# Kernel optimization log

Hardware: AMD Instinct MI355X
Metric: run time of the kernel (lower is better)

Reference implementation:

```python
import jax, jax.numpy as jnp
import numpy as np

# --- fixed physical constants (module params are requires_grad=False) ---
G = 9.81
M = 0.1667
CAF = 5.0 * 0.25 * M * G          # tanh(0) -> ratio = 1.0 exactly
CAR = CAF
LF = 0.09 - 0.036
LR = 0.036
IZ = 0.000267                      # tanh(0) -> pow_ratio = 0 -> Iz_base
THROTTLE_OFFSET = 0.24
THROTTLE_RATIO = 6.98
DT = 0.01
RES_BOUNDS = jnp.array([0.05 * G, 0.05 * G, 0.05 * G * 0.2], dtype=jnp.float32)

B, H, T = 131072, 4, 32


def setup_inputs() -> dict:
    key = jax.random.key(0)
    ks = jax.random.split(key, 8)
    # realistic car states: [x, vx_w, y, vy_w, psi, yaw_rate]
    pos = jax.random.normal(ks[0], (B, H, 2)) * 1.0
    vx = 2.0 + 0.2 * jax.random.normal(ks[1], (B, H, 1))
    vy = 0.1 * jax.random.normal(ks[2], (B, H, 1))
    psi = 0.2 * jax.random.normal(ks[3], (B, H, 1))
    r = 0.1 * jax.random.normal(ks[4], (B, H, 1))
    thr = 0.30 + 0.05 * jax.random.normal(ks[5], (B, H, 1))
    steer = 0.05 * jax.random.normal(ks[6], (B, H, 1))
    full_states = jnp.concatenate(
        [pos[..., :1], vx, pos[..., 1:], vy, psi, r, thr, steer], axis=-1
    ).astype(jnp.float32)
    ka = jax.random.split(ks[7], 6)
    actions = jnp.concatenate(
        [0.30 + 0.05 * jax.random.normal(ka[0], (B, T, 1)),
         0.05 * jax.random.normal(ka[1], (B, T, 1))], axis=-1).astype(jnp.float32)
    in_dim = H * 8
    fc1_w = (jax.random.normal(ka[2], (16, in_dim)) / np.sqrt(in_dim)).astype(jnp.float32)
    fc1_b = (0.01 * jax.random.normal(ka[3], (16,))).astype(jnp.float32)
    fc2_w = (jax.random.normal(ka[4], (3, 16)) / np.sqrt(16)).astype(jnp.float32)
    fc2_b = (0.01 * jax.random.normal(ka[5], (3,))).astype(jnp.float32)
    return {"full_states": full_states, "actions": actions,
            "fc1_w": fc1_w, "fc1_b": fc1_b, "fc2_w": fc2_w, "fc2_b": fc2_b,
            "enable_rnn": 1}


def _rollout(full_states, actions, fc1_w, fc1_b, fc2_w, fc2_b, enable_rnn):
    bsz = full_states.shape[0]
    a33 = lambda Vx: -(2 * CAF + 2 * CAR) / (M * Vx)
    a35 = lambda Vx: -Vx - (2 * CAF * LF - 2 * CAR * LR) / (M * Vx)
    a53 = lambda Vx: -(2 * LF * CAF - 2 * LR * CAR) / (IZ * Vx)
    a55 = lambda Vx: -(2 * LF ** 2 * CAF + 2 * LR ** 2 * CAR) / (IZ * Vx)

    def step(window, act):  # window [B,H,8], act [B,2]
        s = window[:, -1, :6]
        thr, steer = window[:, -1, 6], window[:, -1, 7]
        psi = s[:, 4]
        c, sn = jnp.cos(psi), jnp.sin(psi)
        Vx = s[:, 1] * c + s[:, 3] * sn
        # v = R(-psi) @ s  (body frame)
        v1 = c * s[:, 1] + sn * s[:, 3]
        v3 = -sn * s[:, 1] + c * s[:, 3]
        v5 = s[:, 5]
        long_acc = (thr - THROTTLE_OFFSET) * THROTTLE_RATIO
        # d = A @ v + B @ u
        d0 = v1
        d1 = long_acc
        d2 = v3
        d3 = a33(Vx) * v3 + a35(Vx) * v5 + (2 * CAF / M) * steer
        d4 = v5
        d5 = a53(Vx) * v3 + a55(Vx) * v5 + (2 * LF * CAF / IZ) * steer
        if enable_rnn:
            flat = window.reshape(bsz, -1)
            y1 = jnp.tanh(flat @ fc1_w.T + fc1_b)
            y2 = jnp.tanh(y1 @ fc2_w.T + fc2_b) * RES_BOUNDS[None, :]
            d1 = d1 + y2[:, 0] / M
            d3 = d3 + y2[:, 1] / M
            d5 = d5 + y2[:, 2] / IZ
        # s_new = s + R(psi) @ d * dt
        ns0 = s[:, 0] + (c * d0 - sn * d2) * DT
        ns1 = s[:, 1] + (c * d1 - sn * d3) * DT
        ns2 = s[:, 2] + (sn * d0 + c * d2) * DT
        ns3 = s[:, 3] + (sn * d1 + c * d3) * DT
        ns4 = jnp.mod(s[:, 4] + d4 * DT + jnp.pi, 2 * jnp.pi) - jnp.pi
        ns5 = s[:, 5] + d5 * DT
        new_full = jnp.stack([ns0, ns1, ns2, ns3, ns4, ns5, act[:, 0], act[:, 1]], axis=1)
        new_window = jnp.concatenate([window[:, 1:], new_full[:, None, :]], axis=1)
        return new_window, new_full

    acts_t = jnp.swapaxes(actions, 0, 1)  # [T,B,2]
    _, outs = jax.lax.scan(step, full_states, acts_t)
    return jnp.swapaxes(outs, 0, 1)  # [B,T,8]


def reference(full_states, actions, fc1_w, fc1_b, fc2_w, fc2_b, enable_rnn):
    return _rollout(full_states, actions, fc1_w, fc1_b, fc2_w, fc2_b, bool(enable_rnn))
```

## Files before the change

### kernel.cpp

```cpp
#include <hip/hip_runtime.h>
#include <math.h>

namespace {

typedef short  bf16x8 __attribute__((ext_vector_type(8)));
typedef float  f32x4  __attribute__((ext_vector_type(4)));

constexpr int B_TOTAL = 131072;
constexpr int T_STEPS = 32;

constexpr double dG   = 9.81;
constexpr double dM   = 0.1667;
constexpr double dCAF = 5.0 * 0.25 * dM * dG;
constexpr double dCAR = dCAF;
constexpr double dLF  = 0.09 - 0.036;
constexpr double dLR  = 0.036;
constexpr double dIZ  = 0.000267;

constexpr float A33N = (float)(-(2.0 * dCAF + 2.0 * dCAR));
constexpr float A35N = (float)(-(2.0 * dCAF * dLF - 2.0 * dCAR * dLR));
constexpr float A53N = (float)(-(2.0 * dLF * dCAF - 2.0 * dLR * dCAR));
constexpr float A55N = (float)(-(2.0 * dLF * dLF * dCAF + 2.0 * dLR * dLR * dCAR));
constexpr float ST1  = (float)(2.0 * dCAF / dM);
constexpr float ST5  = (float)(2.0 * dLF * dCAF / dIZ);
constexpr float MF   = (float)dM;
constexpr float IZF  = (float)dIZ;
constexpr float R0M  = (float)(0.05 * dG / dM);
constexpr float R1M  = (float)(0.05 * dG / dM);
constexpr float R2I  = (float)(0.05 * dG * 0.2 / dIZ);
constexpr float THR_OFF = 0.24f;
constexpr float THR_RAT = 6.98f;
constexpr float DT    = 0.01f;
constexpr float PI_F  = (float)3.14159265358979323846;
constexpr float TWOPI = (float)(2.0 * 3.14159265358979323846);
constexpr float INV2PI = (float)(1.0 / (2.0 * 3.14159265358979323846));
constexpr float TWO_LOG2E = 2.8853900817779268f;

__device__ __forceinline__ float fast_tanh(float x) {
    const float e = __builtin_amdgcn_exp2f(x * TWO_LOG2E);
    return fmaf(-2.0f, __builtin_amdgcn_rcpf(e + 1.0f), 1.0f);
}

__device__ __forceinline__ unsigned bf16_rne_u(float f) {
    unsigned u = __float_as_uint(f);
    return (u + 0x7fffu + ((u >> 16) & 1u)) >> 16;
}

__device__ __forceinline__ unsigned pk_bf16(float lo, float hi) {
    unsigned r;
    asm("v_cvt_pk_bf16_f32 %0, %1, %2" : "=v"(r) : "v"(lo), "v"(hi));
    return r;
}
__device__ __forceinline__ float bfl(unsigned p) { return __uint_as_float(p << 16); }
__device__ __forceinline__ float bfh(unsigned p) { return __uint_as_float(p & 0xffff0000u); }

union U4F { uint4 u; bf16x8 f; };

__global__ void prep_kernel(const float* __restrict__ w1, unsigned* __restrict__ ws) {
    const int i = threadIdx.x;
    if (i >= 256) return;
    const int p = i >> 6, L = i & 63;
    const int row = L & 15, g = L >> 4;
    const int pos = (g - p) & 3;
    unsigned hd[4], md[4], ld[4];
    #pragma unroll
    for (int d = 0; d < 4; ++d) {
        unsigned hh[2], mm[2], ll[2];
        #pragma unroll
        for (int s = 0; s < 2; ++s) {
            const float v = w1[row * 32 + pos * 8 + 2 * d + s];
            const unsigned h = bf16_rne_u(v);
            const float r1 = v - __uint_as_float(h << 16);
            const unsigned m = bf16_rne_u(r1);
            const float r2 = r1 - __uint_as_float(m << 16);
            const unsigned l = bf16_rne_u(r2);
            hh[s] = h; mm[s] = m; ll[s] = l;
        }
        hd[d] = hh[0] | (hh[1] << 16);
        md[d] = mm[0] | (mm[1] << 16);
        ld[d] = ll[0] | (ll[1] << 16);
    }
    uint4* w4 = reinterpret_cast<uint4*>(ws);
    w4[(p * 3 + 0) * 64 + L] = make_uint4(hd[0], hd[1], hd[2], hd[3]);
    w4[(p * 3 + 1) * 64 + L] = make_uint4(md[0], md[1], md[2], md[3]);
    w4[(p * 3 + 2) * 64 + L] = make_uint4(ld[0], ld[1], ld[2], ld[3]);
}

__device__ __forceinline__ int xbase(int e) { return (e * 64) ^ ((e & 7) << 4); }

__device__ __forceinline__ void split3_store(
    char* X, int off,
    float v0, float v1, float v2, float v3, float v4, float v5, float v6, float v7)
{
    const unsigned h0 = pk_bf16(v0, v1), h1 = pk_bf16(v2, v3);
    const unsigned h2 = pk_bf16(v4, v5), h3 = pk_bf16(v6, v7);
    const float r0 = v0 - bfl(h0), r1 = v1 - bfh(h0);
    const float r2 = v2 - bfl(h1), r3 = v3 - bfh(h1);
    const float r4 = v4 - bfl(h2), r5 = v5 - bfh(h2);
    const float r6 = v6 - bfl(h3), r7 = v7 - bfh(h3);
    const unsigned m0 = pk_bf16(r0, r1), m1 = pk_bf16(r2, r3);
    const unsigned m2 = pk_bf16(r4, r5), m3 = pk_bf16(r6, r7);
    const unsigned l0 = pk_bf16(r0 - bfl(m0), r1 - bfh(m0));
    const unsigned l1 = pk_bf16(r2 - bfl(m1), r3 - bfh(m1));
    const unsigned l2 = pk_bf16(r4 - bfl(m2), r5 - bfh(m2));
    const unsigned l3 = pk_bf16(r6 - bfl(m3), r7 - bfh(m3));
    *reinterpret_cast<uint4*>(X + off)        = make_uint4(h0, h1, h2, h3);
    *reinterpret_cast<uint4*>(X + 4096 + off) = make_uint4(m0, m1, m2, m3);
    *reinterpret_cast<uint4*>(X + 8192 + off) = make_uint4(l0, l1, l2, l3);
}

__global__ __launch_bounds__(64, 2)
void rollout_kernel(const float* __restrict__ fs,
                    const float* __restrict__ acts,
                    const unsigned* __restrict__ ws,
                    const float* __restrict__ b1g,
                    const float* __restrict__ w2g,
                    const float* __restrict__ b2g,
                    const int*   __restrict__ en,
                    float*       __restrict__ out)
{
    __shared__ char  X[12288];
    __shared__ float abuf[64 * 8];
    __shared__ float sbuf[64 * 16];

    const int L = threadIdx.x;
    const int g = L >> 4;
    const size_t blk = (size_t)blockIdx.x * 64;

    const int rnn = *en;

    bf16x8 Ah[4], Am[4], Al[4];
    {
        const uint4* w4 = reinterpret_cast<const uint4*>(ws);
        #pragma unroll
        for (int p = 0; p < 4; ++p) {
            U4F a; a.u = w4[(p * 3 + 0) * 64 + L]; Ah[p] = a.f;
            U4F b; b.u = w4[(p * 3 + 1) * 64 + L]; Am[p] = b.f;
            U4F c; c.u = w4[(p * 3 + 2) * 64 + L]; Al[p] = c.f;
        }
    }
    float b1s[4];
    #pragma unroll
    for (int r = 0; r < 4; ++r) b1s[r] = b1g[g * 4 + r];
    float w2s[3][4];
    #pragma unroll
    for (int c = 0; c < 3; ++c)
        #pragma unroll
        for (int r = 0; r < 4; ++r) w2s[c][r] = w2g[c * 16 + g * 4 + r];
    const float bias2_0 = b2g[0], bias2_1 = b2g[1], bias2_2 = b2g[2];

    int roffv[4];
    #pragma unroll
    for (int n = 0; n < 4; ++n) roffv[n] = xbase(16 * n + (L & 15)) ^ (g * 16);
    const int wboff = xbase(L);

    const int q0r = L >> 1,        q0f = (L & 1) * 4;
    const int q1r = (64 + L) >> 1, q1f = (L & 1) * 4;
    const int aw0 = q0r * 8 + (q0f ^ (q0r & 4));
    const int aw1 = q1r * 8 + (q1f ^ (q1r & 4));

    float s0, s1, s2, s3, s4, s5, thr, steer;
    {
        const float4* ip = reinterpret_cast<const float4*>(fs + (blk + L) * 32);
        #pragma unroll
        for (int rr = 0; rr < 4; ++rr) {
            const float4 va = ip[rr * 2], vb = ip[rr * 2 + 1];
            split3_store(X, wboff ^ (rr * 16), va.x, va.y, va.z, va.w, vb.x, vb.y, vb.z, vb.w);
            if (rr == 3) {
                s0 = va.x; s1 = va.y; s2 = va.z; s3 = va.w;
                s4 = vb.x; s5 = vb.y; thr = vb.z; steer = vb.w;
            }
        }
    }

    float4 ga0 = *reinterpret_cast<const float4*>(&acts[(blk + q0r) * 64 + q0f]);
    float4 ga1 = *reinterpret_cast<const float4*>(&acts[(blk + q1r) * 64 + q1f]);

    const f32x4 zero4 = {0.f, 0.f, 0.f, 0.f};

    for (int tc = 0; tc < T_STEPS; tc += 4) {
        *reinterpret_cast<float4*>(&abuf[aw0]) = ga0;
        *reinterpret_cast<float4*>(&abuf[aw1]) = ga1;
        const float4 av0 = *reinterpret_cast<const float4*>(&abuf[L * 8 + (0 ^ (L & 4))]);
        const float4 av1 = *reinterpret_cast<const float4*>(&abuf[L * 8 + (4 ^ (L & 4))]);
        if (tc + 4 < T_STEPS) {
            ga0 = *reinterpret_cast<const float4*>(&acts[(blk + q0r) * 64 + (tc + 4) * 2 + q0f]);
            ga1 = *reinterpret_cast<const float4*>(&acts[(blk + q1r) * 64 + (tc + 4) * 2 + q1f]);
        }

        #pragma unroll
        for (int tl = 0; tl < 4; ++tl) {
            const float ax = (tl == 0) ? av0.x : (tl == 1) ? av0.z : (tl == 2) ? av1.x : av1.z;
            const float ay = (tl == 0) ? av0.y : (tl == 1) ? av0.w : (tl == 2) ? av1.y : av1.w;

            const float rev = s4 * INV2PI;
            const float sn = __builtin_amdgcn_sinf(rev);
            const float c  = __builtin_amdgcn_cosf(rev);

            const float Vx = s1 * c + s3 * sn;
            const float v3 = c * s3 - sn * s1;
            const float v5 = s5;

            const float inv_mvx  = __builtin_amdgcn_rcpf(MF * Vx);
            const float inv_izvx = __builtin_amdgcn_rcpf(IZF * Vx);
            const float a33 = A33N * inv_mvx;
            const float a35 = -Vx + A35N * inv_mvx;
            const float a53 = A53N * inv_izvx;
            const float a55 = A55N * inv_izvx;

            const float d0 = Vx;
            float       d1 = (thr - THR_OFF) * THR_RAT;
            const float d2 = v3;
            float       d3 = a33 * v3 + a35 * v5 + ST1 * steer;
            const float d4 = v5;
            float       d5 = a53 * v3 + a55 * v5 + ST5 * steer;

            if (rnn) {
                f32x4 acc[4];
                #pragma unroll
                for (int n = 0; n < 4; ++n) {
                    U4F bh; bh.u = *reinterpret_cast<const uint4*>(X + roffv[n]);
                    U4F bm; bm.u = *reinterpret_cast<const uint4*>(X + 4096 + roffv[n]);
                    U4F bl; bl.u = *reinterpret_cast<const uint4*>(X + 8192 + roffv[n]);
                    f32x4 a = __builtin_amdgcn_mfma_f32_16x16x32_bf16(Ah[tl], bl.f, zero4, 0, 0, 0);
                    a = __builtin_amdgcn_mfma_f32_16x16x32_bf16(Al[tl], bh.f, a, 0, 0, 0);
                    a = __builtin_amdgcn_mfma_f32_16x16x32_bf16(Am[tl], bm.f, a, 0, 0, 0);
                    a = __builtin_amdgcn_mfma_f32_16x16x32_bf16(Am[tl], bh.f, a, 0, 0, 0);
                    a = __builtin_amdgcn_mfma_f32_16x16x32_bf16(Ah[tl], bm.f, a, 0, 0, 0);
                    acc[n] = __builtin_amdgcn_mfma_f32_16x16x32_bf16(Ah[tl], bh.f, a, 0, 0, 0);
                }
                float p0[4], p1[4], p2[4];
                #pragma unroll
                for (int n = 0; n < 4; ++n) {
                    float q0 = 0.f, q1 = 0.f, q2 = 0.f;
                    #pragma unroll
                    for (int r = 0; r < 4; ++r) {
                        const float y = fast_tanh(acc[n][r] + b1s[r]);
                        q0 = fmaf(w2s[0][r], y, q0);
                        q1 = fmaf(w2s[1][r], y, q1);
                        q2 = fmaf(w2s[2][r], y, q2);
                    }
                    p0[n] = q0; p1[n] = q1; p2[n] = q2;
                }
                const bool bb0 = (g & 1) != 0, bb1 = (g & 2) != 0;
                float z0, z1, z2;
                #pragma unroll
                for (int c3 = 0; c3 < 3; ++c3) {
                    const float* p = (c3 == 0) ? p0 : (c3 == 1) ? p1 : p2;
                    const float own = bb1 ? (bb0 ? p[3] : p[2]) : (bb0 ? p[1] : p[0]);
                    const float x1  = bb1 ? (bb0 ? p[2] : p[3]) : (bb0 ? p[0] : p[1]);
                    const float x2  = bb1 ? (bb0 ? p[1] : p[0]) : (bb0 ? p[3] : p[2]);
                    const float x3  = bb1 ? (bb0 ? p[0] : p[1]) : (bb0 ? p[2] : p[3]);
                    const float a = own + __shfl_xor(x1, 16, 64);
                    const float b = x2  + __shfl_xor(x3, 16, 64);
                    const float T = a + __shfl_xor(b, 32, 64);
                    if (c3 == 0) z0 = T; else if (c3 == 1) z1 = T; else z2 = T;
                }
                d1 += fast_tanh(z0 + bias2_0) * R0M;
                d3 += fast_tanh(z1 + bias2_1) * R1M;
                d5 += fast_tanh(z2 + bias2_2) * R2I;
            }

            const float ns0 = s0 + (c * d0 - sn * d2) * DT;
            const float ns1 = s1 + (c * d1 - sn * d3) * DT;
            const float ns2 = s2 + (sn * d0 + c * d2) * DT;
            const float ns3 = s3 + (sn * d1 + c * d3) * DT;
            float aa = s4 + d4 * DT + PI_F;
            aa = aa - floorf(aa * INV2PI) * TWOPI;
            const float ns4 = aa - PI_F;
            const float ns5 = s5 + d5 * DT;

            const int c4b = (tl & 1) * 2;
            *reinterpret_cast<float4*>(&sbuf[L * 16 + 4 * ((c4b + 0) ^ (L & 3))]) =
                make_float4(ns0, ns1, ns2, ns3);
            *reinterpret_cast<float4*>(&sbuf[L * 16 + 4 * ((c4b + 1) ^ (L & 3))]) =
                make_float4(ns4, ns5, ax, ay);

            if (rnn) {
                split3_store(X, wboff ^ (tl * 16), ns0, ns1, ns2, ns3, ns4, ns5, ax, ay);
            }

            s0 = ns0; s1 = ns1; s2 = ns2; s3 = ns3;
            s4 = ns4; s5 = ns5; thr = ax; steer = ay;

            if (tl & 1) {
                const int t2 = tc + tl - 1;
                #pragma unroll
                for (int k = 0; k < 4; ++k) {
                    const int q   = k * 64 + L;
                    const int row = q >> 2;
                    const int f   = q & 3;
                    const float4 v = *reinterpret_cast<const float4*>(
                        &sbuf[row * 16 + 4 * (f ^ (row & 3))]);
                    *reinterpret_cast<float4*>(&out[(blk + row) * 256 + t2 * 8 + f * 4]) = v;
                }
            }
        }
    }
}

}

extern "C" void kernel_launch(void* const* d_in, const int* in_sizes, int n_in,
                              void* d_out, int out_size, void* d_ws, size_t ws_size,
                              hipStream_t stream) {
    const float* fs = (const float*)d_in[0];
    const float* ac = (const float*)d_in[1];
    const float* w1 = (const float*)d_in[2];
    const float* b1 = (const float*)d_in[3];
    const float* w2 = (const float*)d_in[4];
    const float* b2 = (const float*)d_in[5];
    const int*   en = (const int*)d_in[6];
    float* out = (float*)d_out;
    unsigned* ws = (unsigned*)d_ws;

    hipLaunchKernelGGL(prep_kernel, dim3(1), dim3(256), 0, stream, w1, ws);

    dim3 grid(B_TOTAL / 64), block(64);
    hipLaunchKernelGGL(rollout_kernel, grid, block, 0, stream,
                       fs, ac, ws, b1, w2, b2, en, out);
}
```

Before: 73.19 us.

## Halve elements per wave so two lanes share each batch element

Each 64-lane wave now processes 32 batch elements instead of 64. The lane pair for one element duplicates the scalar dynamics and splits the initial LDS fill and the output stores between its two halves. LDS per block shrinks and launch bounds rise to allow more resident waves, with twice as many blocks. This exposes more parallelism and latency hiding for the serial 32-step recurrence and halves the MFMA work per wave. The cost is redundant scalar math across duplicated lanes and less MFMA tile reuse per wave.

```diff
diff --git a/kernel.cpp b/kernel.cpp
--- a/kernel.cpp
+++ b/kernel.cpp
@@ -8,6 +8,7 @@
 
 constexpr int B_TOTAL = 131072;
 constexpr int T_STEPS = 32;
+constexpr int EPW     = 32;
 
 constexpr double dG   = 9.81;
 constexpr double dM   = 0.1667;
@@ -105,11 +106,11 @@
     const unsigned l2 = pk_bf16(r4 - bfl(m2), r5 - bfh(m2));
     const unsigned l3 = pk_bf16(r6 - bfl(m3), r7 - bfh(m3));
     *reinterpret_cast<uint4*>(X + off)        = make_uint4(h0, h1, h2, h3);
-    *reinterpret_cast<uint4*>(X + 4096 + off) = make_uint4(m0, m1, m2, m3);
-    *reinterpret_cast<uint4*>(X + 8192 + off) = make_uint4(l0, l1, l2, l3);
-}
-
-__global__ __launch_bounds__(64, 2)
+    *reinterpret_cast<uint4*>(X + 2048 + off) = make_uint4(m0, m1, m2, m3);
+    *reinterpret_cast<uint4*>(X + 4096 + off) = make_uint4(l0, l1, l2, l3);
+}
+
+__global__ __launch_bounds__(64, 4)
 void rollout_kernel(const float* __restrict__ fs,
                     const float* __restrict__ acts,
                     const unsigned* __restrict__ ws,
@@ -119,13 +120,16 @@
                     const int*   __restrict__ en,
                     float*       __restrict__ out)
 {
-    __shared__ char  X[12288];
-    __shared__ float abuf[64 * 8];
-    __shared__ float sbuf[64 * 16];
+    __shared__ char  X[6144];
+    __shared__ float abuf[EPW * 8];
+    __shared__ float sbuf[EPW * 16];
 
     const int L = threadIdx.x;
     const int g = L >> 4;
-    const size_t blk = (size_t)blockIdx.x * 64;
+    const int e = L & 31;
+    const int h = L >> 5;
+    const bool nb = (g & 1) != 0;
+    const size_t blk = (size_t)blockIdx.x * EPW;
 
     const int rnn = *en;
 
@@ -149,43 +153,41 @@
         for (int r = 0; r < 4; ++r) w2s[c][r] = w2g[c * 16 + g * 4 + r];
     const float bias2_0 = b2g[0], bias2_1 = b2g[1], bias2_2 = b2g[2];
 
-    int roffv[4];
+    int roffv[2];
     #pragma unroll
-    for (int n = 0; n < 4; ++n) roffv[n] = xbase(16 * n + (L & 15)) ^ (g * 16);
-    const int wboff = xbase(L);
-
-    const int q0r = L >> 1,        q0f = (L & 1) * 4;
-    const int q1r = (64 + L) >> 1, q1f = (L & 1) * 4;
+    for (int n = 0; n < 2; ++n) roffv[n] = xbase(16 * n + (L & 15)) ^ (g * 16);
+    const int wboff = xbase(e);
+
+    const int q0r = L >> 1, q0f = (L & 1) * 4;
     const int aw0 = q0r * 8 + (q0f ^ (q0r & 4));
-    const int aw1 = q1r * 8 + (q1f ^ (q1r & 4));
 
     float s0, s1, s2, s3, s4, s5, thr, steer;
     {
-        const float4* ip = reinterpret_cast<const float4*>(fs + (blk + L) * 32);
-        #pragma unroll
-        for (int rr = 0; rr < 4; ++rr) {
-            const float4 va = ip[rr * 2], vb = ip[rr * 2 + 1];
-            split3_store(X, wboff ^ (rr * 16), va.x, va.y, va.z, va.w, vb.x, vb.y, vb.z, vb.w);
-            if (rr == 3) {
-                s0 = va.x; s1 = va.y; s2 = va.z; s3 = va.w;
-                s4 = vb.x; s5 = vb.y; thr = vb.z; steer = vb.w;
-            }
-        }
+        const float4* ip = reinterpret_cast<const float4*>(fs + (blk + e) * 32);
+        const float4 r3a = ip[6], r3b = ip[7];
+        if (h == 0) {
+            const float4 a0 = ip[0], b0 = ip[1], a1 = ip[2], b1 = ip[3];
+            split3_store(X, wboff ^ 0,  a0.x, a0.y, a0.z, a0.w, b0.x, b0.y, b0.z, b0.w);
+            split3_store(X, wboff ^ 16, a1.x, a1.y, a1.z, a1.w, b1.x, b1.y, b1.z, b1.w);
+        } else {
+            const float4 a2 = ip[4], b2 = ip[5];
+            split3_store(X, wboff ^ 32, a2.x, a2.y, a2.z, a2.w, b2.x, b2.y, b2.z, b2.w);
+            split3_store(X, wboff ^ 48, r3a.x, r3a.y, r3a.z, r3a.w, r3b.x, r3b.y, r3b.z, r3b.w);
+        }
+        s0 = r3a.x; s1 = r3a.y; s2 = r3a.z; s3 = r3a.w;
+        s4 = r3b.x; s5 = r3b.y; thr = r3b.z; steer = r3b.w;
     }
 
     float4 ga0 = *reinterpret_cast<const float4*>(&acts[(blk + q0r) * 64 + q0f]);
-    float4 ga1 = *reinterpret_cast<const float4*>(&acts[(blk + q1r) * 64 + q1f]);
 
     const f32x4 zero4 = {0.f, 0.f, 0.f, 0.f};
 
     for (int tc = 0; tc < T_STEPS; tc += 4) {
         *reinterpret_cast<float4*>(&abuf[aw0]) = ga0;
-        *reinterpret_cast<float4*>(&abuf[aw1]) = ga1;
-        const float4 av0 = *reinterpret_cast<const float4*>(&abuf[L * 8 + (0 ^ (L & 4))]);
-        const float4 av1 = *reinterpret_cast<const float4*>(&abuf[L * 8 + (4 ^ (L & 4))]);
+        const float4 av0 = *reinterpret_cast<const float4*>(&abuf[e * 8 + (0 ^ (e & 4))]);
+        const float4 av1 = *reinterpret_cast<const float4*>(&abuf[e * 8 + (4 ^ (e & 4))]);
         if (tc + 4 < T_STEPS) {
             ga0 = *reinterpret_cast<const float4*>(&acts[(blk + q0r) * 64 + (tc + 4) * 2 + q0f]);
-            ga1 = *reinterpret_cast<const float4*>(&acts[(blk + q1r) * 64 + (tc + 4) * 2 + q1f]);
         }
 
         #pragma unroll
@@ -216,12 +218,12 @@
             float       d5 = a53 * v3 + a55 * v5 + ST5 * steer;
 
             if (rnn) {
-                f32x4 acc[4];
+                f32x4 acc[2];
                 #pragma unroll
-                for (int n = 0; n < 4; ++n) {
+                for (int n = 0; n < 2; ++n) {
                     U4F bh; bh.u = *reinterpret_cast<const uint4*>(X + roffv[n]);
-                    U4F bm; bm.u = *reinterpret_cast<const uint4*>(X + 4096 + roffv[n]);
-                    U4F bl; bl.u = *reinterpret_cast<const uint4*>(X + 8192 + roffv[n]);
+                    U4F bm; bm.u = *reinterpret_cast<const uint4*>(X + 2048 + roffv[n]);
+                    U4F bl; bl.u = *reinterpret_cast<const uint4*>(X + 4096 + roffv[n]);
                     f32x4 a = __builtin_amdgcn_mfma_f32_16x16x32_bf16(Ah[tl], bl.f, zero4, 0, 0, 0);
                     a = __builtin_amdgcn_mfma_f32_16x16x32_bf16(Al[tl], bh.f, a, 0, 0, 0);
                     a = __builtin_amdgcn_mfma_f32_16x16x32_bf16(Am[tl], bm.f, a, 0, 0, 0);
@@ -229,9 +231,9 @@
                     a = __builtin_amdgcn_mfma_f32_16x16x32_bf16(Ah[tl], bm.f, a, 0, 0, 0);
                     acc[n] = __builtin_amdgcn_mfma_f32_16x16x32_bf16(Ah[tl], bh.f, a, 0, 0, 0);
                 }
-                float p0[4], p1[4], p2[4];
+                float p0[2], p1[2], p2[2];
                 #pragma unroll
-                for (int n = 0; n < 4; ++n) {
+                for (int n = 0; n < 2; ++n) {
                     float q0 = 0.f, q1 = 0.f, q2 = 0.f;
                     #pragma unroll
                     for (int r = 0; r < 4; ++r) {
@@ -242,18 +244,14 @@
                     }
                     p0[n] = q0; p1[n] = q1; p2[n] = q2;
                 }
-                const bool bb0 = (g & 1) != 0, bb1 = (g & 2) != 0;
                 float z0, z1, z2;
                 #pragma unroll
                 for (int c3 = 0; c3 < 3; ++c3) {
                     const float* p = (c3 == 0) ? p0 : (c3 == 1) ? p1 : p2;
-                    const float own = bb1 ? (bb0 ? p[3] : p[2]) : (bb0 ? p[1] : p[0]);
-                    const float x1  = bb1 ? (bb0 ? p[2] : p[3]) : (bb0 ? p[0] : p[1]);
-                    const float x2  = bb1 ? (bb0 ? p[1] : p[0]) : (bb0 ? p[3] : p[2]);
-                    const float x3  = bb1 ? (bb0 ? p[0] : p[1]) : (bb0 ? p[2] : p[3]);
-                    const float a = own + __shfl_xor(x1, 16, 64);
-                    const float b = x2  + __shfl_xor(x3, 16, 64);
-                    const float T = a + __shfl_xor(b, 32, 64);
+                    const float own  = nb ? p[1] : p[0];
+                    const float sent = nb ? p[0] : p[1];
+                    const float a = own + __shfl_xor(sent, 16, 64);
+                    const float T = a + __shfl_xor(a, 32, 64);
                     if (c3 == 0) z0 = T; else if (c3 == 1) z1 = T; else z2 = T;
                 }
                 d1 += fast_tanh(z0 + bias2_0) * R0M;
@@ -271,13 +269,14 @@
             const float ns5 = s5 + d5 * DT;
 
             const int c4b = (tl & 1) * 2;
-            *reinterpret_cast<float4*>(&sbuf[L * 16 + 4 * ((c4b + 0) ^ (L & 3))]) =
-                make_float4(ns0, ns1, ns2, ns3);
-            *reinterpret_cast<float4*>(&sbuf[L * 16 + 4 * ((c4b + 1) ^ (L & 3))]) =
-                make_float4(ns4, ns5, ax, ay);
+            const float4 vout = h ? make_float4(ns4, ns5, ax, ay)
+                                  : make_float4(ns0, ns1, ns2, ns3);
+            *reinterpret_cast<float4*>(&sbuf[e * 16 + 4 * ((c4b + h) ^ (e & 3))]) = vout;
 
             if (rnn) {
-                split3_store(X, wboff ^ (tl * 16), ns0, ns1, ns2, ns3, ns4, ns5, ax, ay);
+                if (h == 0) {
+                    split3_store(X, wboff ^ (tl * 16), ns0, ns1, ns2, ns3, ns4, ns5, ax, ay);
+                }
             }
 
             s0 = ns0; s1 = ns1; s2 = ns2; s3 = ns3;
@@ -286,7 +285,7 @@
             if (tl & 1) {
                 const int t2 = tc + tl - 1;
                 #pragma unroll
-                for (int k = 0; k < 4; ++k) {
+                for (int k = 0; k < 2; ++k) {
                     const int q   = k * 64 + L;
                     const int row = q >> 2;
                     const int f   = q & 3;
@@ -316,7 +315,7 @@
 
     hipLaunchKernelGGL(prep_kernel, dim3(1), dim3(256), 0, stream, w1, ws);
 
-    dim3 grid(B_TOTAL / 64), block(64);
+    dim3 grid(B_TOTAL / EPW), block(64);
     hipLaunchKernelGGL(rollout_kernel, grid, block, 0, stream,
                        fs, ac, ws, b1, w2, b2, en, out);
 }
```

Result: slower. 88.50 us (+20.9%).
